# Optimization experiments

Measured on AMD Instinct MI355X. Metric: run time of the kernel, lower is better.

## Reference

```python
import jax, jax.numpy as jnp
import numpy as np

EPS = 1e-5  # BatchNorm eps (torch default)
K = 16      # num_neighbors


def _bn(x, gamma, beta, axes):
    # training-mode BatchNorm (biased variance), channel axis = 1
    mu = x.mean(axes, keepdims=True)
    var = x.var(axes, keepdims=True)
    shp = [1] * x.ndim
    shp[1] = -1
    return (x - mu) * jax.lax.rsqrt(var + EPS) * gamma.reshape(shp) + beta.reshape(shp)


def setup_inputs() -> dict:
    key = jax.random.key(0)
    ks = jax.random.split(key, 6)
    B, C, N, E = 4, 3, 4096, 256
    s = lambda k_, shp, fan: jax.random.normal(k_, shp, jnp.float32) * np.float32(1.0 / np.sqrt(fan))
    return {
        "x": jax.random.normal(ks[0], (B, C, N), jnp.float32),
        "g1": jnp.ones((C,), jnp.float32), "b1": jnp.zeros((C,), jnp.float32),
        "W1": s(ks[1], (E, C), C), "bw1": jnp.zeros((E,), jnp.float32),
        "g2a": jnp.ones((C,), jnp.float32), "b2a": jnp.zeros((C,), jnp.float32),
        "W2a": s(ks[2], (E, C), C),
        "g2b": jnp.ones((E,), jnp.float32), "b2b": jnp.zeros((E,), jnp.float32),
        "W2b": s(ks[3], (E, E), E),
        "Wf": s(ks[4], (E, 2 * E), 2 * E), "bf": jnp.zeros((E,), jnp.float32),
    }


def reference(x, g1, b1, W1, bw1, g2a, b2a, W2a, g2b, b2b, W2b, Wf, bf):
    B, C, N = x.shape
    xn = _bn(x, g1, b1, (0, 2))                               # BatchNorm1d
    point_emb = jnp.einsum('ec,bcn->ben', W1, xn) + bw1[None, :, None]  # conv1 (1x1)
    # dist = -||xi - xj||; torch topk(dist, largest=False) picks the K LARGEST
    # distances. Squared distance is monotone in the norm, so top_k on d2 gives
    # identical indices without materializing [B,3,N,N].
    x2 = jnp.sum(xn * xn, axis=1)                             # [B,N]
    d2 = x2[:, :, None] + x2[:, None, :] - 2.0 * jnp.einsum('bcn,bcm->bnm', xn, xn)
    _, idx = jax.lax.top_k(d2, min(K, N))                     # [B,N,K]
    idx = idx[:, :, 1:]                                       # original loop skips index 0
    gathered = jax.vmap(lambda xb, ib: xb[:, ib])(xn, idx)    # [B,C,N,K-1]
    neigh = gathered - xn[:, :, :, None]                      # edge features
    h = _bn(neigh, g2a, b2a, (0, 2, 3))                       # BatchNorm2d(Cin)
    h = jnp.einsum('ec,bcnk->benk', W2a, h)                   # 1x1 conv, no bias
    h = jax.nn.gelu(_bn(h, g2b, b2b, (0, 2, 3)), approximate=False)
    h = jnp.einsum('fe,benk->bfnk', W2b, h)                   # 1x1 conv, no bias
    neigh_emb = h.max(-1)                                     # max over neighbors
    feat = jnp.concatenate([point_emb, neigh_emb], axis=1)    # [B,2E,N]
    return jnp.einsum('of,bfn->bon', Wf, feat) + bf[None, :, None]
```

## Files before the change

kernel.cpp:

```cpp
#include <hip/hip_runtime.h>
#include <float.h>
#include <math.h>

#define EPS 1e-5f
constexpr int B = 4, C = 3, N = 4096, E = 256;
constexpr int KNN = 15;
constexpr int BN_ = B * N;
constexpr int P = 8;
constexpr int SR  = 264;
constexpr int SRF = 520;

typedef short bf8 __attribute__((ext_vector_type(8)));
typedef float f4  __attribute__((ext_vector_type(4)));

static __device__ __forceinline__ unsigned short f2bf(float f) {
    union { float f; unsigned int u; } v; v.f = f;
    unsigned int r = v.u + 0x7FFFu + ((v.u >> 16) & 1u);
    return (unsigned short)(r >> 16);
}
static __device__ __forceinline__ unsigned int pkbf(float a, float b) {
    unsigned int r;
    asm("v_cvt_pk_bf16_f32 %0, %1, %2" : "=v"(r) : "v"(a), "v"(b));
    return r;
}
static __device__ __forceinline__ bf8 ld_bf8(const unsigned short* p) {
    return *(const bf8*)p;
}
static __device__ __forceinline__ float gelu_t(float v) {
    float z = v * fmaf(v * v, 0.07135482f, 1.59576912f);
    float r = __builtin_amdgcn_rcpf(1.f + __expf(z));
    return fmaf(-v, r, v);
}

template <int CTRL>
static __device__ __forceinline__ float dppmax(float x) {
    int xi = __float_as_int(x);
    int yi = __builtin_amdgcn_update_dpp(xi, xi, CTRL, 0xF, 0xF, false);
    return fmaxf(x, __int_as_float(yi));
}
static __device__ __forceinline__ float wave_max_bcast(float x) {
    x = dppmax<0x111>(x);
    x = dppmax<0x112>(x);
    x = dppmax<0x114>(x);
    x = dppmax<0x118>(x);
    x = dppmax<0x142>(x);
    x = dppmax<0x143>(x);
    return __int_as_float(__builtin_amdgcn_readlane(__float_as_int(x), 63));
}

__global__ void bn1_stats(const float* __restrict__ x, float* __restrict__ bn1,
                          float* __restrict__ S9) {
    int c = blockIdx.x, t = threadIdx.x;
    if (c == C) {
        for (int u = t; u < 64 * 9; u += 256) S9[u] = 0.f;
        return;
    }
    float s = 0.f, ss = 0.f;
    for (int i4 = t; i4 < BN_ / 4; i4 += 256) {
        int b = i4 >> 10, n4 = i4 & 1023;
        float4 v = ((const float4*)(x + (b * C + c) * N))[n4];
        s += v.x + v.y + v.z + v.w;
        ss += v.x * v.x + v.y * v.y + v.z * v.z + v.w * v.w;
    }
    __shared__ float rs_[256], rss_[256];
    rs_[t] = s; rss_[t] = ss; __syncthreads();
    for (int w = 128; w > 0; w >>= 1) {
        if (t < w) { rs_[t] += rs_[t + w]; rss_[t] += rss_[t + w]; }
        __syncthreads();
    }
    if (t == 0) {
        float mu = rs_[0] / (float)BN_;
        float var = rss_[0] / (float)BN_ - mu * mu;
        bn1[c] = mu; bn1[3 + c] = rsqrtf(var + EPS);
    }
}

__global__ void compute_xn_cvt(const float* __restrict__ x,
                               const float* __restrict__ g1,
                               const float* __restrict__ b1,
                               const float* __restrict__ bn1,
                               float4* __restrict__ xn4,
                               const float* __restrict__ W2b, const float* __restrict__ Wf,
                               unsigned short* __restrict__ w2b_t, unsigned short* __restrict__ wf_t) {
    int blk = blockIdx.x;
    if (blk < BN_ / 256) {
        int i = blk * 256 + threadIdx.x;
        int b = i >> 12, n = i & (N - 1);
        float v[3];
        #pragma unroll
        for (int c = 0; c < C; c++)
            v[c] = (x[(b * C + c) * N + n] - bn1[c]) * bn1[3 + c] * g1[c] + b1[c];
        float4 o; o.x = v[0]; o.y = v[1]; o.z = v[2];
        o.w = v[0] * v[0] + v[1] * v[1] + v[2] * v[2];
        xn4[i] = o;
        return;
    }
    int ch = (blk - BN_ / 256) * 256 + threadIdx.x;
    if (ch < 8192) {
        int lane = ch & 63, kb = (ch >> 6) & 7, ft16 = ch >> 9;
        int row = ft16 * 16 + (lane & 15);
        int col = kb * 32 + (lane >> 4) * 8;
        #pragma unroll
        for (int j = 0; j < 8; j++)
            w2b_t[ch * 8 + j] = f2bf(W2b[row * 256 + col + j]);
    } else {
        int c2 = ch - 8192;
        int lane = c2 & 63, kb = (c2 >> 6) & 15, ot = c2 >> 10;
        int row = ot * 16 + (lane & 15);
        int col = kb * 32 + (lane >> 4) * 8;
        #pragma unroll
        for (int j = 0; j < 8; j++)
            wf_t[c2 * 8 + j] = f2bf(Wf[row * 512 + col + j]);
    }
}

__global__ void __launch_bounds__(256, 4) knn_kernel(const float4* __restrict__ xn4,
                                                     unsigned short* __restrict__ idxout,
                                                     float* __restrict__ S9) {
    __shared__ float smom[4][15][9];
    __shared__ float ptx[1024], pty[1024], ptz[1024], ptw[1024];
    int w = threadIdx.x >> 6, lane = threadIdx.x & 63;
    int i = blockIdx.x * 4 + w;
    int b = i >> 12, n = i & (N - 1);
    const float4* xb = xn4 + b * N;
    float4 qv = xb[n];
    float d[64];
    #pragma unroll
    for (int ch = 0; ch < 4; ch++) {
        if (ch) __syncthreads();
        #pragma unroll
        for (int u = 0; u < 4; u++) {
            int s = u * 256 + threadIdx.x;
            float4 v = xb[ch * 1024 + s];
            ptx[s] = v.x; pty[s] = v.y; ptz[s] = v.z; ptw[s] = v.w;
        }
        __syncthreads();
        #pragma unroll
        for (int j = 0; j < 16; j++) {
            int s = j * 64 + lane;
            d[ch * 16 + j] = qv.w + ptw[s]
                - 2.f * (qv.x * ptx[s] + qv.y * pty[s] + qv.z * ptz[s]);
        }
    }
    float cm[8];
    #pragma unroll
    for (int c = 0; c < 8; c++) {
        float v = d[c * 8];
        #pragma unroll
        for (int s = 1; s < 8; s++) v = fmaxf(v, d[c * 8 + s]);
        cm[c] = v;
    }
    float bv = cm[0];
    #pragma unroll
    for (int c = 1; c < 8; c++) bv = fmaxf(bv, cm[c]);

    int myj = 0;
    for (int r = 0; r < 16; r++) {
        float wv = wave_max_bcast(bv);
        unsigned long long msk = __ballot(bv == wv);
        int wl = __ffsll(msk) - 1;
        int gi = 0;
        if (lane == wl) {
            int cstar = 0; bool got = false;
            #pragma unroll
            for (int c = 0; c < 8; c++) {
                bool h = !got && (cm[c] == bv);
                cstar = h ? c : cstar;
                got = got || h;
            }
            int slot = 0;
            #pragma unroll
            for (int c = 0; c < 8; c++) {
                if (c == cstar) {
                    bool g2 = false;
                    #pragma unroll
                    for (int s = 0; s < 8; s++) {
                        bool h = !g2 && (d[c * 8 + s] == bv);
                        slot = h ? (c * 8 + s) : slot;
                        g2 = g2 || h;
                    }
                    #pragma unroll
                    for (int s = 0; s < 8; s++)
                        d[c * 8 + s] = (c * 8 + s == slot) ? -FLT_MAX : d[c * 8 + s];
                    float v = d[c * 8];
                    #pragma unroll
                    for (int s = 1; s < 8; s++) v = fmaxf(v, d[c * 8 + s]);
                    cm[c] = v;
                }
            }
            bv = cm[0];
            #pragma unroll
            for (int c = 1; c < 8; c++) bv = fmaxf(bv, cm[c]);
            gi = slot * 64 + lane;
        }
        int g = __shfl(gi, wl);
        if (lane == r - 1) myj = g;
    }

    bool act = lane < 15;
    if (act) idxout[i * KNN + lane] = (unsigned short)myj;
    float4 pj = xb[act ? myj : n];
    float v0 = pj.x - qv.x, v1 = pj.y - qv.y, v2 = pj.z - qv.z;
    if (act) {
        float* mm = smom[w][lane];
        mm[0] = v0; mm[1] = v1; mm[2] = v2;
        mm[3] = v0 * v0; mm[4] = v1 * v1; mm[5] = v2 * v2;
        mm[6] = v0 * v1; mm[7] = v0 * v2; mm[8] = v1 * v2;
    }
    __syncthreads();
    int t = threadIdx.x;
    if (t < 36) {
        int wsel = t / 9, j = t % 9;
        float a = 0.f;
        #pragma unroll
        for (int u = 0; u < 15; u++) a += smom[wsel][u][j];
        atomicAdd(&S9[((blockIdx.x * 4 + wsel) & 63) * 9 + j], a);
    }
}

__global__ void finalize_stats(const float* __restrict__ S9,
                               const float* __restrict__ g2a, const float* __restrict__ b2a,
                               const float* __restrict__ W2a,
                               const float* __restrict__ g2b, const float* __restrict__ b2b,
                               float* __restrict__ ab, float4* __restrict__ wsb) {
    const float cnt = (float)(BN_ * KNN);
    __shared__ float S[9];
    __shared__ float alpha[3], beta[3], mu[3], Ehh[3][3];
    int t = threadIdx.x;
    if (t < 9) {
        float a = 0.f;
        for (int u = 0; u < 64; u++) a += S9[u * 9 + t];
        S[t] = a;
    }
    __syncthreads();
    if (t == 0) {
        float m[3];
        float s2[3][3];
        s2[0][0] = S[3]; s2[1][1] = S[4]; s2[2][2] = S[5];
        s2[0][1] = s2[1][0] = S[6]; s2[0][2] = s2[2][0] = S[7]; s2[1][2] = s2[2][1] = S[8];
        for (int c = 0; c < 3; c++) {
            m[c] = S[c] / cnt;
            float var = s2[c][c] / cnt - m[c] * m[c];
            alpha[c] = g2a[c] * rsqrtf(var + EPS);
            beta[c]  = b2a[c] - m[c] * alpha[c];
            mu[c] = m[c];
            ab[c] = alpha[c]; ab[3 + c] = beta[c];
        }
        for (int c = 0; c < 3; c++)
            for (int cc = 0; cc < 3; cc++)
                Ehh[c][cc] = alpha[c] * alpha[cc] * (s2[c][cc] / cnt)
                           + alpha[c] * beta[cc] * m[c]
                           + beta[c] * alpha[cc] * m[cc]
                           + beta[c] * beta[cc];
    }
    __syncthreads();
    int e = t;
    float wv[3], Eh[3];
    for (int c = 0; c < 3; c++) { wv[c] = W2a[e * 3 + c]; Eh[c] = alpha[c] * mu[c] + beta[c]; }
    float mean = wv[0] * Eh[0] + wv[1] * Eh[1] + wv[2] * Eh[2];
    float m2 = 0.f;
    for (int c = 0; c < 3; c++)
        for (int cc = 0; cc < 3; cc++) m2 += wv[c] * wv[cc] * Ehh[c][cc];
    float var = m2 - mean * mean;
    float s = g2b[e] * rsqrtf(var + EPS);
    float4 o;
    o.x = wv[0] * s; o.y = wv[1] * s; o.z = wv[2] * s; o.w = b2b[e] - mean * s;
    wsb[e] = o;
}

__global__ void __launch_bounds__(512, 2) fused_final(
        const float4* __restrict__ xn4, const unsigned short* __restrict__ idx,
        const float* __restrict__ ab,
        const float4* __restrict__ wsb,
        const unsigned short* __restrict__ w2b_t,
        const float* __restrict__ W1, const float* __restrict__ bw1,
        const unsigned short* __restrict__ wf_t, const float* __restrict__ bfv,
        float* __restrict__ out) {
    __shared__ __align__(16) unsigned short hh_bf[2][64 * SR];
    __shared__ __align__(16) unsigned short feat_bf[8 * SRF];
    __shared__ __align__(16) float4 hhat4[P][16];
    int i0 = blockIdx.x * P;
    int t = threadIdx.x;
    int b = i0 >> 12, n0 = i0 & (N - 1);
    const float4* xb = xn4 + b * N;

    int w = t >> 6, lane = t & 63;
    int m = lane & 15, q = lane >> 4;

    auto phaseB = [&](int pg) {
        int ep = t & 127;
        int pq = t >> 7;
        int p  = pg * 4 + pq;
        float4 wA = wsb[2 * ep];
        float4 wB = wsb[2 * ep + 1];
        float g0A = 0.f, g0B = 0.f;
        #pragma unroll
        for (int k = 0; k < KNN; k++) {
            float4 hv = hhat4[p][k];
            float vA = fmaf(wA.x, hv.x, fmaf(wA.y, hv.y, fmaf(wA.z, hv.z, wA.w)));
            float vB = fmaf(wB.x, hv.x, fmaf(wB.y, hv.y, fmaf(wB.z, hv.z, wB.w)));
            float gA = gelu_t(vA), gB = gelu_t(vB);
            *(unsigned int*)&hh_bf[pg][(16 * pq + k) * SR + 2 * ep] = pkbf(gA, gB);
            if (k == 0) { g0A = gA; g0B = gB; }
        }
        *(unsigned int*)&hh_bf[pg][(16 * pq + 15) * SR + 2 * ep] = pkbf(g0A, g0B);
        float4 pv = xb[n0 + p];
        float peA = bw1[2 * ep] + W1[(2 * ep) * 3] * pv.x
                  + W1[(2 * ep) * 3 + 1] * pv.y + W1[(2 * ep) * 3 + 2] * pv.z;
        float peB = bw1[2 * ep + 1] + W1[(2 * ep + 1) * 3] * pv.x
                  + W1[(2 * ep + 1) * 3 + 1] * pv.y + W1[(2 * ep + 1) * 3 + 2] * pv.z;
        *(unsigned int*)&feat_bf[p * SRF + 2 * ep] = pkbf(peA, peB);
    };

    auto phaseC = [&](int pg) {
        bf8 a0[8], a1[8];
        #pragma unroll
        for (int kb = 0; kb < 8; kb++) {
            a0[kb] = ld_bf8(w2b_t + (w * 2 + 0) * 4096 + kb * 512 + lane * 8);
            a1[kb] = ld_bf8(w2b_t + (w * 2 + 1) * 4096 + kb * 512 + lane * 8);
        }
        #pragma unroll 1
        for (int pp = 0; pp < 4; pp++) {
            bf8 hfr[8];
            #pragma unroll
            for (int kb = 0; kb < 8; kb++)
                hfr[kb] = ld_bf8(&hh_bf[pg][(16 * pp + m) * SR + kb * 32 + q * 8]);
            f4 acc0 = {0.f, 0.f, 0.f, 0.f};
            f4 acc1 = {0.f, 0.f, 0.f, 0.f};
            #pragma unroll
            for (int kb = 0; kb < 8; kb++) {
                acc0 = __builtin_amdgcn_mfma_f32_16x16x32_bf16(hfr[kb], a0[kb], acc0, 0, 0, 0);
                acc1 = __builtin_amdgcn_mfma_f32_16x16x32_bf16(hfr[kb], a1[kb], acc1, 0, 0, 0);
            }
            float mx0 = fmaxf(fmaxf(acc0[0], acc0[1]), fmaxf(acc0[2], acc0[3]));
            float mx1 = fmaxf(fmaxf(acc1[0], acc1[1]), fmaxf(acc1[2], acc1[3]));
            mx0 = fmaxf(mx0, __shfl_xor(mx0, 16));
            mx0 = fmaxf(mx0, __shfl_xor(mx0, 32));
            mx1 = fmaxf(mx1, __shfl_xor(mx1, 16));
            mx1 = fmaxf(mx1, __shfl_xor(mx1, 32));
            if (lane < 16) {
                feat_bf[(pg * 4 + pp) * SRF + E + (w * 2 + 0) * 16 + lane] = f2bf(mx0);
                feat_bf[(pg * 4 + pp) * SRF + E + (w * 2 + 1) * 16 + lane] = f2bf(mx1);
            }
        }
    };

    if (t < P * KNN) {
        int p = t / KNN, k = t % KNN;
        int j = idx[(i0 + p) * KNN + k];
        float4 pj = xb[j];
        float4 pn = xb[n0 + p];
        float4 h;
        h.x = ab[0] * (pj.x - pn.x) + ab[3];
        h.y = ab[1] * (pj.y - pn.y) + ab[4];
        h.z = ab[2] * (pj.z - pn.z) + ab[5];
        h.w = 0.f;
        hhat4[p][k] = h;
    }
    __syncthreads();

    phaseB(0);
    __syncthreads();

    phaseB(1);
    phaseC(0);
    __syncthreads();

    phaseC(1);
    __syncthreads();

    {
        bf8 fb[16];
        #pragma unroll
        for (int kb = 0; kb < 16; kb++)
            fb[kb] = ld_bf8(&feat_bf[(m & 7) * SRF + kb * 32 + q * 8]);
        #pragma unroll
        for (int o2 = 0; o2 < 2; o2++) {
            int ot = w * 2 + o2;
            f4 acc = {0.f, 0.f, 0.f, 0.f};
            #pragma unroll
            for (int kb = 0; kb < 16; kb++) {
                bf8 a = ld_bf8(wf_t + ot * 8192 + kb * 512 + lane * 8);
                acc = __builtin_amdgcn_mfma_f32_16x16x32_bf16(a, fb[kb], acc, 0, 0, 0);
            }
            if (m < P) {
                int o0 = ot * 16 + 4 * q;
                out[(b * E + o0 + 0) * N + n0 + m] = acc[0] + bfv[o0 + 0];
                out[(b * E + o0 + 1) * N + n0 + m] = acc[1] + bfv[o0 + 1];
                out[(b * E + o0 + 2) * N + n0 + m] = acc[2] + bfv[o0 + 2];
                out[(b * E + o0 + 3) * N + n0 + m] = acc[3] + bfv[o0 + 3];
            }
        }
    }
}

extern "C" void kernel_launch(void* const* d_in, const int* in_sizes, int n_in,
                              void* d_out, int out_size, void* d_ws, size_t ws_size,
                              hipStream_t stream) {
    (void)in_sizes; (void)n_in; (void)out_size; (void)ws_size;
    const float* x   = (const float*)d_in[0];
    const float* g1  = (const float*)d_in[1];
    const float* b1  = (const float*)d_in[2];
    const float* W1  = (const float*)d_in[3];
    const float* bw1 = (const float*)d_in[4];
    const float* g2a = (const float*)d_in[5];
    const float* b2a = (const float*)d_in[6];
    const float* W2a = (const float*)d_in[7];
    const float* g2b = (const float*)d_in[8];
    const float* b2b = (const float*)d_in[9];
    const float* W2b = (const float*)d_in[10];
    const float* Wf  = (const float*)d_in[11];
    const float* bfv = (const float*)d_in[12];
    float* out = (float*)d_out;

    char* ws = (char*)d_ws;
    size_t off = 0;
    auto alloc = [&](size_t bytes) { size_t o = off; off = (off + bytes + 255) & ~(size_t)255; return o; };
    float4* xn4           = (float4*)(ws + alloc(sizeof(float4) * BN_));
    unsigned short* idx   = (unsigned short*)(ws + alloc(sizeof(unsigned short) * BN_ * KNN));
    float* bn1            = (float*)(ws + alloc(sizeof(float) * 8));
    float* S9             = (float*)(ws + alloc(sizeof(float) * 64 * 9));
    float* ab             = (float*)(ws + alloc(sizeof(float) * 8));
    float4* wsb           = (float4*)(ws + alloc(sizeof(float4) * E));
    unsigned short* w2bt  = (unsigned short*)(ws + alloc(sizeof(unsigned short) * E * E));
    unsigned short* wft   = (unsigned short*)(ws + alloc(sizeof(unsigned short) * E * 2 * E));

    bn1_stats<<<C + 1, 256, 0, stream>>>(x, bn1, S9);
    compute_xn_cvt<<<BN_ / 256 + (8192 + 16384) / 256, 256, 0, stream>>>(
        x, g1, b1, bn1, xn4, W2b, Wf, w2bt, wft);
    knn_kernel<<<BN_ / 4, 256, 0, stream>>>(xn4, idx, S9);
    finalize_stats<<<1, 256, 0, stream>>>(S9, g2a, b2a, W2a, g2b, b2b, ab, wsb);
    fused_final<<<BN_ / P, 512, 0, stream>>>(xn4, idx, ab, wsb, w2bt, W1, bw1, wft, bfv, out);
}
```

Before: 218.1 us.

## Fuse prep kernels, recompute normalized points inline, fold finalize stats into final kernel

Merges BN1 stats, S9 zeroing and weight conversion into one prep kernel. Drops the xn4 intermediate, so KNN and the final kernel now normalize x on the fly. The separate finalize_stats launch is folded into fused_final, where every block recomputes the BN2 coefficients. The final Wf GEMM is split into two halves around a barrier. This removes two launches and a global round trip, at the cost of redundant per-block stats math and extra strided loads of x.

```diff
diff --git a/kernel.cpp b/kernel.cpp
--- a/kernel.cpp
+++ b/kernel.cpp
@@ -48,54 +48,39 @@
     return __int_as_float(__builtin_amdgcn_readlane(__float_as_int(x), 63));
 }
 
-__global__ void bn1_stats(const float* __restrict__ x, float* __restrict__ bn1,
-                          float* __restrict__ S9) {
-    int c = blockIdx.x, t = threadIdx.x;
-    if (c == C) {
+__global__ void prep_kernel(const float* __restrict__ x,
+                            const float* __restrict__ g1, const float* __restrict__ b1,
+                            float* __restrict__ bn1, float* __restrict__ S9,
+                            const float* __restrict__ W2b, const float* __restrict__ Wf,
+                            unsigned short* __restrict__ w2b_t, unsigned short* __restrict__ wf_t) {
+    int blk = blockIdx.x, t = threadIdx.x;
+    if (blk < C) {
+        int c = blk;
+        float s = 0.f, ss = 0.f;
+        for (int i4 = t; i4 < BN_ / 4; i4 += 256) {
+            int b = i4 >> 10, n4 = i4 & 1023;
+            float4 v = ((const float4*)(x + (b * C + c) * N))[n4];
+            s += v.x + v.y + v.z + v.w;
+            ss += v.x * v.x + v.y * v.y + v.z * v.z + v.w * v.w;
+        }
+        __shared__ float rs_[256], rss_[256];
+        rs_[t] = s; rss_[t] = ss; __syncthreads();
+        for (int w = 128; w > 0; w >>= 1) {
+            if (t < w) { rs_[t] += rs_[t + w]; rss_[t] += rss_[t + w]; }
+            __syncthreads();
+        }
+        if (t == 0) {
+            float mu = rs_[0] / (float)BN_;
+            float var = rss_[0] / (float)BN_ - mu * mu;
+            bn1[c] = mu; bn1[3 + c] = rsqrtf(var + EPS);
+        }
+        return;
+    }
+    if (blk == C) {
         for (int u = t; u < 64 * 9; u += 256) S9[u] = 0.f;
         return;
     }
-    float s = 0.f, ss = 0.f;
-    for (int i4 = t; i4 < BN_ / 4; i4 += 256) {
-        int b = i4 >> 10, n4 = i4 & 1023;
-        float4 v = ((const float4*)(x + (b * C + c) * N))[n4];
-        s += v.x + v.y + v.z + v.w;
-        ss += v.x * v.x + v.y * v.y + v.z * v.z + v.w * v.w;
-    }
-    __shared__ float rs_[256], rss_[256];
-    rs_[t] = s; rss_[t] = ss; __syncthreads();
-    for (int w = 128; w > 0; w >>= 1) {
-        if (t < w) { rs_[t] += rs_[t + w]; rss_[t] += rss_[t + w]; }
-        __syncthreads();
-    }
-    if (t == 0) {
-        float mu = rs_[0] / (float)BN_;
-        float var = rss_[0] / (float)BN_ - mu * mu;
-        bn1[c] = mu; bn1[3 + c] = rsqrtf(var + EPS);
-    }
-}
-
-__global__ void compute_xn_cvt(const float* __restrict__ x,
-                               const float* __restrict__ g1,
-                               const float* __restrict__ b1,
-                               const float* __restrict__ bn1,
-                               float4* __restrict__ xn4,
-                               const float* __restrict__ W2b, const float* __restrict__ Wf,
-                               unsigned short* __restrict__ w2b_t, unsigned short* __restrict__ wf_t) {
-    int blk = blockIdx.x;
-    if (blk < BN_ / 256) {
-        int i = blk * 256 + threadIdx.x;
-        int b = i >> 12, n = i & (N - 1);
-        float v[3];
-        #pragma unroll
-        for (int c = 0; c < C; c++)
-            v[c] = (x[(b * C + c) * N + n] - bn1[c]) * bn1[3 + c] * g1[c] + b1[c];
-        float4 o; o.x = v[0]; o.y = v[1]; o.z = v[2];
-        o.w = v[0] * v[0] + v[1] * v[1] + v[2] * v[2];
-        xn4[i] = o;
-        return;
-    }
-    int ch = (blk - BN_ / 256) * 256 + threadIdx.x;
+    int ch = (blk - C - 1) * 256 + t;
     if (ch < 8192) {
         int lane = ch & 63, kb = (ch >> 6) & 7, ft16 = ch >> 9;
         int row = ft16 * 16 + (lane & 15);
@@ -114,7 +99,10 @@
     }
 }
 
-__global__ void __launch_bounds__(256, 4) knn_kernel(const float4* __restrict__ xn4,
+__global__ void __launch_bounds__(256, 4) knn_kernel(const float* __restrict__ x,
+                                                     const float* __restrict__ bn1g,
+                                                     const float* __restrict__ g1,
+                                                     const float* __restrict__ b1,
                                                      unsigned short* __restrict__ idxout,
                                                      float* __restrict__ S9) {
     __shared__ float smom[4][15][9];
@@ -122,8 +110,17 @@
     int w = threadIdx.x >> 6, lane = threadIdx.x & 63;
     int i = blockIdx.x * 4 + w;
     int b = i >> 12, n = i & (N - 1);
-    const float4* xb = xn4 + b * N;
-    float4 qv = xb[n];
+    const float* xp0 = x + (b * C + 0) * N;
+    const float* xp1 = x + (b * C + 1) * N;
+    const float* xp2 = x + (b * C + 2) * N;
+    float mu0 = bn1g[0], mu1 = bn1g[1], mu2 = bn1g[2];
+    float r0 = bn1g[3], r1 = bn1g[4], r2 = bn1g[5];
+    float G0 = g1[0], G1 = g1[1], G2 = g1[2];
+    float Bb0 = b1[0], Bb1 = b1[1], Bb2 = b1[2];
+    float qx = (xp0[n] - mu0) * r0 * G0 + Bb0;
+    float qy = (xp1[n] - mu1) * r1 * G1 + Bb1;
+    float qz = (xp2[n] - mu2) * r2 * G2 + Bb2;
+    float qw = qx * qx + qy * qy + qz * qz;
     float d[64];
     #pragma unroll
     for (int ch = 0; ch < 4; ch++) {
@@ -131,15 +128,19 @@
         #pragma unroll
         for (int u = 0; u < 4; u++) {
             int s = u * 256 + threadIdx.x;
-            float4 v = xb[ch * 1024 + s];
-            ptx[s] = v.x; pty[s] = v.y; ptz[s] = v.z; ptw[s] = v.w;
+            int g = ch * 1024 + s;
+            float v0 = (xp0[g] - mu0) * r0 * G0 + Bb0;
+            float v1 = (xp1[g] - mu1) * r1 * G1 + Bb1;
+            float v2 = (xp2[g] - mu2) * r2 * G2 + Bb2;
+            ptx[s] = v0; pty[s] = v1; ptz[s] = v2;
+            ptw[s] = v0 * v0 + v1 * v1 + v2 * v2;
         }
         __syncthreads();
         #pragma unroll
         for (int j = 0; j < 16; j++) {
             int s = j * 64 + lane;
-            d[ch * 16 + j] = qv.w + ptw[s]
-                - 2.f * (qv.x * ptx[s] + qv.y * pty[s] + qv.z * ptz[s]);
+            d[ch * 16 + j] = qw + ptw[s]
+                - 2.f * (qx * ptx[s] + qy * pty[s] + qz * ptz[s]);
         }
     }
     float cm[8];
@@ -199,8 +200,11 @@
 
     bool act = lane < 15;
     if (act) idxout[i * KNN + lane] = (unsigned short)myj;
-    float4 pj = xb[act ? myj : n];
-    float v0 = pj.x - qv.x, v1 = pj.y - qv.y, v2 = pj.z - qv.z;
+    int jj = act ? myj : n;
+    float pjx = (xp0[jj] - mu0) * r0 * G0 + Bb0;
+    float pjy = (xp1[jj] - mu1) * r1 * G1 + Bb1;
+    float pjz = (xp2[jj] - mu2) * r2 * G2 + Bb2;
+    float v0 = pjx - qx, v1 = pjy - qy, v2 = pjz - qz;
     if (act) {
         float* mm = smom[w][lane];
         mm[0] = v0; mm[1] = v1; mm[2] = v2;
@@ -218,33 +222,52 @@
     }
 }
 
-__global__ void finalize_stats(const float* __restrict__ S9,
-                               const float* __restrict__ g2a, const float* __restrict__ b2a,
-                               const float* __restrict__ W2a,
-                               const float* __restrict__ g2b, const float* __restrict__ b2b,
-                               float* __restrict__ ab, float4* __restrict__ wsb) {
+__global__ void __launch_bounds__(512, 2) fused_final(
+        const float* __restrict__ x, const unsigned short* __restrict__ idx,
+        const float* __restrict__ S9,
+        const float* __restrict__ g2a, const float* __restrict__ b2a,
+        const float* __restrict__ W2a,
+        const float* __restrict__ g2b, const float* __restrict__ b2b,
+        const unsigned short* __restrict__ w2b_t,
+        const float* __restrict__ W1, const float* __restrict__ bw1,
+        const unsigned short* __restrict__ wf_t, const float* __restrict__ bfv,
+        const float* __restrict__ bn1g, const float* __restrict__ g1,
+        const float* __restrict__ b1,
+        float* __restrict__ out) {
+    __shared__ __align__(16) unsigned short hh_bf[2][64 * SR];
+    __shared__ __align__(16) unsigned short feat_bf[8 * SRF];
+    __shared__ __align__(16) float4 hhat4[P][16];
+    __shared__ float S_[9];
+    __shared__ float alpha[3], beta[3], muv[3], Ehh[3][3], ab_sh[6];
+    __shared__ float xnp_sh[8][3];
+    int i0 = blockIdx.x * P;
+    int t = threadIdx.x;
+    int b = i0 >> 12, n0 = i0 & (N - 1);
+
     const float cnt = (float)(BN_ * KNN);
-    __shared__ float S[9];
-    __shared__ float alpha[3], beta[3], mu[3], Ehh[3][3];
-    int t = threadIdx.x;
     if (t < 9) {
         float a = 0.f;
         for (int u = 0; u < 64; u++) a += S9[u * 9 + t];
-        S[t] = a;
+        S_[t] = a;
+    }
+    if (t >= 64 && t < 88) {
+        int p = (t - 64) / 3, c = (t - 64) % 3;
+        float xv = x[(b * C + c) * N + n0 + p];
+        xnp_sh[p][c] = (xv - bn1g[c]) * bn1g[3 + c] * g1[c] + b1[c];
     }
     __syncthreads();
     if (t == 0) {
         float m[3];
         float s2[3][3];
-        s2[0][0] = S[3]; s2[1][1] = S[4]; s2[2][2] = S[5];
-        s2[0][1] = s2[1][0] = S[6]; s2[0][2] = s2[2][0] = S[7]; s2[1][2] = s2[2][1] = S[8];
+        s2[0][0] = S_[3]; s2[1][1] = S_[4]; s2[2][2] = S_[5];
+        s2[0][1] = s2[1][0] = S_[6]; s2[0][2] = s2[2][0] = S_[7]; s2[1][2] = s2[2][1] = S_[8];
         for (int c = 0; c < 3; c++) {
-            m[c] = S[c] / cnt;
+            m[c] = S_[c] / cnt;
             float var = s2[c][c] / cnt - m[c] * m[c];
             alpha[c] = g2a[c] * rsqrtf(var + EPS);
             beta[c]  = b2a[c] - m[c] * alpha[c];
-            mu[c] = m[c];
-            ab[c] = alpha[c]; ab[3 + c] = beta[c];
+            muv[c] = m[c];
+            ab_sh[c] = alpha[c]; ab_sh[3 + c] = beta[c];
         }
         for (int c = 0; c < 3; c++)
             for (int cc = 0; cc < 3; cc++)
@@ -254,35 +277,38 @@
                            + beta[c] * beta[cc];
     }
     __syncthreads();
-    int e = t;
-    float wv[3], Eh[3];
-    for (int c = 0; c < 3; c++) { wv[c] = W2a[e * 3 + c]; Eh[c] = alpha[c] * mu[c] + beta[c]; }
-    float mean = wv[0] * Eh[0] + wv[1] * Eh[1] + wv[2] * Eh[2];
-    float m2 = 0.f;
-    for (int c = 0; c < 3; c++)
-        for (int cc = 0; cc < 3; cc++) m2 += wv[c] * wv[cc] * Ehh[c][cc];
-    float var = m2 - mean * mean;
-    float s = g2b[e] * rsqrtf(var + EPS);
-    float4 o;
-    o.x = wv[0] * s; o.y = wv[1] * s; o.z = wv[2] * s; o.w = b2b[e] - mean * s;
-    wsb[e] = o;
-}
-
-__global__ void __launch_bounds__(512, 2) fused_final(
-        const float4* __restrict__ xn4, const unsigned short* __restrict__ idx,
-        const float* __restrict__ ab,
-        const float4* __restrict__ wsb,
-        const unsigned short* __restrict__ w2b_t,
-        const float* __restrict__ W1, const float* __restrict__ bw1,
-        const unsigned short* __restrict__ wf_t, const float* __restrict__ bfv,
-        float* __restrict__ out) {
-    __shared__ __align__(16) unsigned short hh_bf[2][64 * SR];
-    __shared__ __align__(16) unsigned short feat_bf[8 * SRF];
-    __shared__ __align__(16) float4 hhat4[P][16];
-    int i0 = blockIdx.x * P;
-    int t = threadIdx.x;
-    int b = i0 >> 12, n0 = i0 & (N - 1);
-    const float4* xb = xn4 + b * N;
+
+    int ep0 = t & 127;
+    auto mk_wsb = [&](int e) -> float4 {
+        float wv[3], Eh[3];
+        for (int c = 0; c < 3; c++) { wv[c] = W2a[e * 3 + c]; Eh[c] = alpha[c] * muv[c] + beta[c]; }
+        float mean = wv[0] * Eh[0] + wv[1] * Eh[1] + wv[2] * Eh[2];
+        float m2 = 0.f;
+        for (int c = 0; c < 3; c++)
+            for (int cc = 0; cc < 3; cc++) m2 += wv[c] * wv[cc] * Ehh[c][cc];
+        float var = m2 - mean * mean;
+        float s = g2b[e] * rsqrtf(var + EPS);
+        float4 o;
+        o.x = wv[0] * s; o.y = wv[1] * s; o.z = wv[2] * s; o.w = b2b[e] - mean * s;
+        return o;
+    };
+    float4 wA = mk_wsb(2 * ep0);
+    float4 wB = mk_wsb(2 * ep0 + 1);
+
+    if (t < P * KNN) {
+        int p = t / KNN, k = t % KNN;
+        int j = idx[(i0 + p) * KNN + k];
+        float xnj0 = (x[(b * C + 0) * N + j] - bn1g[0]) * bn1g[3] * g1[0] + b1[0];
+        float xnj1 = (x[(b * C + 1) * N + j] - bn1g[1]) * bn1g[4] * g1[1] + b1[1];
+        float xnj2 = (x[(b * C + 2) * N + j] - bn1g[2]) * bn1g[5] * g1[2] + b1[2];
+        float4 h;
+        h.x = ab_sh[0] * (xnj0 - xnp_sh[p][0]) + ab_sh[3];
+        h.y = ab_sh[1] * (xnj1 - xnp_sh[p][1]) + ab_sh[4];
+        h.z = ab_sh[2] * (xnj2 - xnp_sh[p][2]) + ab_sh[5];
+        h.w = 0.f;
+        hhat4[p][k] = h;
+    }
+    __syncthreads();
 
     int w = t >> 6, lane = t & 63;
     int m = lane & 15, q = lane >> 4;
@@ -291,8 +317,6 @@
         int ep = t & 127;
         int pq = t >> 7;
         int p  = pg * 4 + pq;
-        float4 wA = wsb[2 * ep];
-        float4 wB = wsb[2 * ep + 1];
         float g0A = 0.f, g0B = 0.f;
         #pragma unroll
         for (int k = 0; k < KNN; k++) {
@@ -304,11 +328,11 @@
             if (k == 0) { g0A = gA; g0B = gB; }
         }
         *(unsigned int*)&hh_bf[pg][(16 * pq + 15) * SR + 2 * ep] = pkbf(g0A, g0B);
-        float4 pv = xb[n0 + p];
-        float peA = bw1[2 * ep] + W1[(2 * ep) * 3] * pv.x
-                  + W1[(2 * ep) * 3 + 1] * pv.y + W1[(2 * ep) * 3 + 2] * pv.z;
-        float peB = bw1[2 * ep + 1] + W1[(2 * ep + 1) * 3] * pv.x
-                  + W1[(2 * ep + 1) * 3 + 1] * pv.y + W1[(2 * ep + 1) * 3 + 2] * pv.z;
+        float pvx = xnp_sh[p][0], pvy = xnp_sh[p][1], pvz = xnp_sh[p][2];
+        float peA = bw1[2 * ep] + W1[(2 * ep) * 3] * pvx
+                  + W1[(2 * ep) * 3 + 1] * pvy + W1[(2 * ep) * 3 + 2] * pvz;
+        float peB = bw1[2 * ep + 1] + W1[(2 * ep + 1) * 3] * pvx
+                  + W1[(2 * ep + 1) * 3 + 1] * pvy + W1[(2 * ep + 1) * 3 + 2] * pvz;
         *(unsigned int*)&feat_bf[p * SRF + 2 * ep] = pkbf(peA, peB);
     };
 
@@ -345,20 +369,6 @@
         }
     };
 
-    if (t < P * KNN) {
-        int p = t / KNN, k = t % KNN;
-        int j = idx[(i0 + p) * KNN + k];
-        float4 pj = xb[j];
-        float4 pn = xb[n0 + p];
-        float4 h;
-        h.x = ab[0] * (pj.x - pn.x) + ab[3];
-        h.y = ab[1] * (pj.y - pn.y) + ab[4];
-        h.z = ab[2] * (pj.z - pn.z) + ab[5];
-        h.w = 0.f;
-        hhat4[p][k] = h;
-    }
-    __syncthreads();
-
     phaseB(0);
     __syncthreads();
 
@@ -366,30 +376,53 @@
     phaseC(0);
     __syncthreads();
 
+    f4 accD0 = {0.f, 0.f, 0.f, 0.f};
+    f4 accD1 = {0.f, 0.f, 0.f, 0.f};
     phaseC(1);
-    __syncthreads();
-
     {
-        bf8 fb[16];
-        #pragma unroll
-        for (int kb = 0; kb < 16; kb++)
-            fb[kb] = ld_bf8(&feat_bf[(m & 7) * SRF + kb * 32 + q * 8]);
-        #pragma unroll
-        for (int o2 = 0; o2 < 2; o2++) {
-            int ot = w * 2 + o2;
-            f4 acc = {0.f, 0.f, 0.f, 0.f};
-            #pragma unroll
-            for (int kb = 0; kb < 16; kb++) {
-                bf8 a = ld_bf8(wf_t + ot * 8192 + kb * 512 + lane * 8);
-                acc = __builtin_amdgcn_mfma_f32_16x16x32_bf16(a, fb[kb], acc, 0, 0, 0);
-            }
-            if (m < P) {
-                int o0 = ot * 16 + 4 * q;
-                out[(b * E + o0 + 0) * N + n0 + m] = acc[0] + bfv[o0 + 0];
-                out[(b * E + o0 + 1) * N + n0 + m] = acc[1] + bfv[o0 + 1];
-                out[(b * E + o0 + 2) * N + n0 + m] = acc[2] + bfv[o0 + 2];
-                out[(b * E + o0 + 3) * N + n0 + m] = acc[3] + bfv[o0 + 3];
-            }
+        bf8 fb8[8];
+        #pragma unroll
+        for (int k2 = 0; k2 < 8; k2++)
+            fb8[k2] = ld_bf8(&feat_bf[(m & 7) * SRF + k2 * 32 + q * 8]);
+        #pragma unroll
+        for (int k2 = 0; k2 < 8; k2++) {
+            bf8 aa = ld_bf8(wf_t + (w * 2 + 0) * 8192 + k2 * 512 + lane * 8);
+            accD0 = __builtin_amdgcn_mfma_f32_16x16x32_bf16(aa, fb8[k2], accD0, 0, 0, 0);
+        }
+        #pragma unroll
+        for (int k2 = 0; k2 < 8; k2++) {
+            bf8 aa = ld_bf8(wf_t + (w * 2 + 1) * 8192 + k2 * 512 + lane * 8);
+            accD1 = __builtin_amdgcn_mfma_f32_16x16x32_bf16(aa, fb8[k2], accD1, 0, 0, 0);
+        }
+    }
+    __syncthreads();
+
+    {
+        bf8 fb8[8];
+        #pragma unroll
+        for (int k2 = 0; k2 < 8; k2++)
+            fb8[k2] = ld_bf8(&feat_bf[(m & 7) * SRF + (8 + k2) * 32 + q * 8]);
+        #pragma unroll
+        for (int k2 = 0; k2 < 8; k2++) {
+            bf8 aa = ld_bf8(wf_t + (w * 2 + 0) * 8192 + (8 + k2) * 512 + lane * 8);
+            accD0 = __builtin_amdgcn_mfma_f32_16x16x32_bf16(aa, fb8[k2], accD0, 0, 0, 0);
+        }
+        #pragma unroll
+        for (int k2 = 0; k2 < 8; k2++) {
+            bf8 aa = ld_bf8(wf_t + (w * 2 + 1) * 8192 + (8 + k2) * 512 + lane * 8);
+            accD1 = __builtin_amdgcn_mfma_f32_16x16x32_bf16(aa, fb8[k2], accD1, 0, 0, 0);
+        }
+        if (m < P) {
+            int o0 = (w * 2 + 0) * 16 + 4 * q;
+            out[(b * E + o0 + 0) * N + n0 + m] = accD0[0] + bfv[o0 + 0];
+            out[(b * E + o0 + 1) * N + n0 + m] = accD0[1] + bfv[o0 + 1];
+            out[(b * E + o0 + 2) * N + n0 + m] = accD0[2] + bfv[o0 + 2];
+            out[(b * E + o0 + 3) * N + n0 + m] = accD0[3] + bfv[o0 + 3];
+            int o1 = (w * 2 + 1) * 16 + 4 * q;
+            out[(b * E + o1 + 0) * N + n0 + m] = accD1[0] + bfv[o1 + 0];
+            out[(b * E + o1 + 1) * N + n0 + m] = accD1[1] + bfv[o1 + 1];
+            out[(b * E + o1 + 2) * N + n0 + m] = accD1[2] + bfv[o1 + 2];
+            out[(b * E + o1 + 3) * N + n0 + m] = accD1[3] + bfv[o1 + 3];
         }
     }
 }
@@ -416,19 +449,15 @@
     char* ws = (char*)d_ws;
     size_t off = 0;
     auto alloc = [&](size_t bytes) { size_t o = off; off = (off + bytes + 255) & ~(size_t)255; return o; };
-    float4* xn4           = (float4*)(ws + alloc(sizeof(float4) * BN_));
     unsigned short* idx   = (unsigned short*)(ws + alloc(sizeof(unsigned short) * BN_ * KNN));
     float* bn1            = (float*)(ws + alloc(sizeof(float) * 8));
     float* S9             = (float*)(ws + alloc(sizeof(float) * 64 * 9));
-    float* ab             = (float*)(ws + alloc(sizeof(float) * 8));
-    float4* wsb           = (float4*)(ws + alloc(sizeof(float4) * E));
     unsigned short* w2bt  = (unsigned short*)(ws + alloc(sizeof(unsigned short) * E * E));
     unsigned short* wft   = (unsigned short*)(ws + alloc(sizeof(unsigned short) * E * 2 * E));
 
-    bn1_stats<<<C + 1, 256, 0, stream>>>(x, bn1, S9);
-    compute_xn_cvt<<<BN_ / 256 + (8192 + 16384) / 256, 256, 0, stream>>>(
-        x, g1, b1, bn1, xn4, W2b, Wf, w2bt, wft);
-    knn_kernel<<<BN_ / 4, 256, 0, stream>>>(xn4, idx, S9);
-    finalize_stats<<<1, 256, 0, stream>>>(S9, g2a, b2a, W2a, g2b, b2b, ab, wsb);
-    fused_final<<<BN_ / P, 512, 0, stream>>>(xn4, idx, ab, wsb, w2bt, W1, bw1, wft, bfv, out);
-}
+    prep_kernel<<<C + 1 + (8192 + 16384) / 256, 256, 0, stream>>>(
+        x, g1, b1, bn1, S9, W2b, Wf, w2bt, wft);
+    knn_kernel<<<BN_ / 4, 256, 0, stream>>>(x, bn1, g1, b1, idx, S9);
+    fused_final<<<BN_ / P, 512, 0, stream>>>(
+        x, idx, S9, g2a, b2a, W2a, g2b, b2b, w2bt, W1, bw1, wft, bfv, bn1, g1, b1, out);
+}
```

Measured after the change: 226.4 us. 3.8% more time.

## Overlap final projection with last phase and use float4 shared points in kNN

Applied to the files above, without the earlier changes.

The final Wf projection is split into two K-halves. The first half (point embedding features, already available) runs right after phaseC(1) issues, before the barrier, so MFMA work overlaps the tail of the last phase. The second half runs after the barrier. The kNN kernel also stores the staged point tile as one float4 shared array instead of four scalar arrays, so each candidate is a single vector LDS load. This relies on phaseC(1) writing only the upper half of feat_bf, and the float4 layout may cause more LDS bank conflicts per access.

```diff
diff --git a/kernel.cpp b/kernel.cpp
--- a/kernel.cpp
+++ b/kernel.cpp
@@ -118,7 +118,7 @@
                                                      unsigned short* __restrict__ idxout,
                                                      float* __restrict__ S9) {
     __shared__ float smom[4][15][9];
-    __shared__ float ptx[1024], pty[1024], ptz[1024], ptw[1024];
+    __shared__ __align__(16) float4 pts[1024];
     int w = threadIdx.x >> 6, lane = threadIdx.x & 63;
     int i = blockIdx.x * 4 + w;
     int b = i >> 12, n = i & (N - 1);
@@ -129,17 +129,13 @@
     for (int ch = 0; ch < 4; ch++) {
         if (ch) __syncthreads();
         #pragma unroll
-        for (int u = 0; u < 4; u++) {
-            int s = u * 256 + threadIdx.x;
-            float4 v = xb[ch * 1024 + s];
-            ptx[s] = v.x; pty[s] = v.y; ptz[s] = v.z; ptw[s] = v.w;
-        }
+        for (int u = 0; u < 4; u++)
+            pts[u * 256 + threadIdx.x] = xb[ch * 1024 + u * 256 + threadIdx.x];
         __syncthreads();
         #pragma unroll
         for (int j = 0; j < 16; j++) {
-            int s = j * 64 + lane;
-            d[ch * 16 + j] = qv.w + ptw[s]
-                - 2.f * (qv.x * ptx[s] + qv.y * pty[s] + qv.z * ptz[s]);
+            float4 p = pts[j * 64 + lane];
+            d[ch * 16 + j] = qv.w + p.w - 2.f * (qv.x * p.x + qv.y * p.y + qv.z * p.z);
         }
     }
     float cm[8];
@@ -366,30 +362,53 @@
     phaseC(0);
     __syncthreads();
 
+    f4 accD0 = {0.f, 0.f, 0.f, 0.f};
+    f4 accD1 = {0.f, 0.f, 0.f, 0.f};
     phaseC(1);
-    __syncthreads();
-
     {
-        bf8 fb[16];
-        #pragma unroll
-        for (int kb = 0; kb < 16; kb++)
-            fb[kb] = ld_bf8(&feat_bf[(m & 7) * SRF + kb * 32 + q * 8]);
-        #pragma unroll
-        for (int o2 = 0; o2 < 2; o2++) {
-            int ot = w * 2 + o2;
-            f4 acc = {0.f, 0.f, 0.f, 0.f};
-            #pragma unroll
-            for (int kb = 0; kb < 16; kb++) {
-                bf8 a = ld_bf8(wf_t + ot * 8192 + kb * 512 + lane * 8);
-                acc = __builtin_amdgcn_mfma_f32_16x16x32_bf16(a, fb[kb], acc, 0, 0, 0);
-            }
-            if (m < P) {
-                int o0 = ot * 16 + 4 * q;
-                out[(b * E + o0 + 0) * N + n0 + m] = acc[0] + bfv[o0 + 0];
-                out[(b * E + o0 + 1) * N + n0 + m] = acc[1] + bfv[o0 + 1];
-                out[(b * E + o0 + 2) * N + n0 + m] = acc[2] + bfv[o0 + 2];
-                out[(b * E + o0 + 3) * N + n0 + m] = acc[3] + bfv[o0 + 3];
-            }
+        bf8 fb8[8];
+        #pragma unroll
+        for (int k2 = 0; k2 < 8; k2++)
+            fb8[k2] = ld_bf8(&feat_bf[(m & 7) * SRF + k2 * 32 + q * 8]);
+        #pragma unroll
+        for (int k2 = 0; k2 < 8; k2++) {
+            bf8 aa = ld_bf8(wf_t + (w * 2 + 0) * 8192 + k2 * 512 + lane * 8);
+            accD0 = __builtin_amdgcn_mfma_f32_16x16x32_bf16(aa, fb8[k2], accD0, 0, 0, 0);
+        }
+        #pragma unroll
+        for (int k2 = 0; k2 < 8; k2++) {
+            bf8 aa = ld_bf8(wf_t + (w * 2 + 1) * 8192 + k2 * 512 + lane * 8);
+            accD1 = __builtin_amdgcn_mfma_f32_16x16x32_bf16(aa, fb8[k2], accD1, 0, 0, 0);
+        }
+    }
+    __syncthreads();
+
+    {
+        bf8 fb8[8];
+        #pragma unroll
+        for (int k2 = 0; k2 < 8; k2++)
+            fb8[k2] = ld_bf8(&feat_bf[(m & 7) * SRF + (8 + k2) * 32 + q * 8]);
+        #pragma unroll
+        for (int k2 = 0; k2 < 8; k2++) {
+            bf8 aa = ld_bf8(wf_t + (w * 2 + 0) * 8192 + (8 + k2) * 512 + lane * 8);
+            accD0 = __builtin_amdgcn_mfma_f32_16x16x32_bf16(aa, fb8[k2], accD0, 0, 0, 0);
+        }
+        #pragma unroll
+        for (int k2 = 0; k2 < 8; k2++) {
+            bf8 aa = ld_bf8(wf_t + (w * 2 + 1) * 8192 + (8 + k2) * 512 + lane * 8);
+            accD1 = __builtin_amdgcn_mfma_f32_16x16x32_bf16(aa, fb8[k2], accD1, 0, 0, 0);
+        }
+        if (m < P) {
+            int o0 = (w * 2 + 0) * 16 + 4 * q;
+            out[(b * E + o0 + 0) * N + n0 + m] = accD0[0] + bfv[o0 + 0];
+            out[(b * E + o0 + 1) * N + n0 + m] = accD0[1] + bfv[o0 + 1];
+            out[(b * E + o0 + 2) * N + n0 + m] = accD0[2] + bfv[o0 + 2];
+            out[(b * E + o0 + 3) * N + n0 + m] = accD0[3] + bfv[o0 + 3];
+            int o1 = (w * 2 + 1) * 16 + 4 * q;
+            out[(b * E + o1 + 0) * N + n0 + m] = accD1[0] + bfv[o1 + 0];
+            out[(b * E + o1 + 1) * N + n0 + m] = accD1[1] + bfv[o1 + 1];
+            out[(b * E + o1 + 2) * N + n0 + m] = accD1[2] + bfv[o1 + 2];
+            out[(b * E + o1 + 3) * N + n0 + m] = accD1[3] + bfv[o1 + 3];
         }
     }
 }
```

Measured after the change: 221.5 us. Within noise of the previous version (+1.6%).
